# Kernel tuning notes

Hardware: AMD Instinct MI355X
Metric: run time of the kernel (lower is better)

## Reference

```python
import jax, jax.numpy as jnp
import numpy as np
from jax import lax

B, S, I = 256, 16, 64
D = 128
N_ITEMS = 100000
K = 3
PAD_ID = 0
BOS_ID = N_ITEMS
DILATIONS = (1, 2, 4)


def setup_inputs() -> dict:
    key = jax.random.key(0)
    ks = jax.random.split(key, 16)
    item_id = jax.random.randint(ks[0], (B, S, I), 0, N_ITEMS, dtype=jnp.int32)
    eval_from = jax.random.randint(ks[1], (B,), 0, S, dtype=jnp.int32)
    u_type = jax.random.randint(ks[2], (B,), 0, 4, dtype=jnp.int32)
    emb = jax.random.normal(ks[3], (N_ITEMS + 1, D), jnp.float32) * 0.05
    emb = emb.at[PAD_ID].set(0.0)  # padding_idx=0
    kaiming = (2.0 / (D * K)) ** 0.5
    conv_w0 = jax.random.normal(ks[4], (D, D, K), jnp.float32) * kaiming
    conv_w1 = jax.random.normal(ks[5], (D, D, K), jnp.float32) * kaiming
    conv_w2 = jax.random.normal(ks[6], (D, D, K), jnp.float32) * kaiming
    conv_b0 = jnp.zeros((D,), jnp.float32)
    conv_b1 = jnp.zeros((D,), jnp.float32)
    conv_b2 = jnp.zeros((D,), jnp.float32)
    gru_wih = jax.random.normal(ks[7], (3 * D, D), jnp.float32) * 0.05
    gru_whh = jax.random.normal(ks[8], (3 * D, D), jnp.float32) * 0.05
    gru_bih = jax.random.normal(ks[9], (3 * D,), jnp.float32) * 0.05
    gru_bhh = jax.random.normal(ks[10], (3 * D,), jnp.float32) * 0.05
    fus_w = jax.random.normal(ks[11], (D, 2 * D), jnp.float32) * 0.05
    fus_b = jnp.zeros((D,), jnp.float32)
    return {"item_id": item_id, "eval_from": eval_from, "u_type": u_type,
            "emb": emb,
            "conv_w0": conv_w0, "conv_b0": conv_b0,
            "conv_w1": conv_w1, "conv_b1": conv_b1,
            "conv_w2": conv_w2, "conv_b2": conv_b2,
            "gru_wih": gru_wih, "gru_whh": gru_whh,
            "gru_bih": gru_bih, "gru_bhh": gru_bhh,
            "fus_w": fus_w, "fus_b": fus_b}


def reference(item_id, eval_from, u_type, emb,
              conv_w0, conv_b0, conv_w1, conv_b1, conv_w2, conv_b2,
              gru_wih, gru_whh, gru_bih, gru_bhh, fus_w, fus_b):
    item_id = jnp.maximum(item_id, 0)  # clamp_min(0)
    Bc, Sc, Ic = item_id.shape
    convs = ((conv_w0, conv_b0, DILATIONS[0]),
             (conv_w1, conv_b1, DILATIONS[1]),
             (conv_w2, conv_b2, DILATIONS[2]))

    def tcn(x):  # x: [B, T, D] -> [B, T, D]
        h = jnp.transpose(x, (0, 2, 1))  # NCH
        for w, b, dil in convs:
            pad = (K - 1) * dil
            out = lax.conv_general_dilated(
                h, w, window_strides=(1,), padding=[(pad, 0)],
                rhs_dilation=(dil,),
                dimension_numbers=('NCH', 'OIH', 'NCH')) + b[None, :, None]
            h = jax.nn.relu(out + h)
        return jnp.transpose(h, (0, 2, 1))

    def gru_step(h, x):  # h,x: [B, D]
        gi = x @ gru_wih.T + gru_bih
        gh = h @ gru_whh.T + gru_bhh
        ir, iz, inn = jnp.split(gi, 3, axis=-1)
        hr, hz, hn = jnp.split(gh, 3, axis=-1)
        r = jax.nn.sigmoid(ir + hr)
        z = jax.nn.sigmoid(iz + hz)
        n = jnp.tanh(inn + r * hn)
        return (1.0 - z) * n + z * h

    pos = jnp.arange(Ic + 1)
    bos = jnp.full((Bc, 1), BOS_ID, dtype=item_id.dtype)

    def step(h, seq_s):  # seq_s: [B, I]
        lengths = (seq_s != PAD_ID).sum(-1)          # [B]
        max_len = lengths.max()                       # batch-level session max
        seq = jnp.concatenate([bos, seq_s], axis=1)   # [B, I+1], BOS prepended
        valid = pos[None, :] <= max_len               # positions torch keeps
        seq = jnp.where(valid, seq, PAD_ID)
        mask = seq != PAD_ID
        e = emb[seq]                                  # [B, I+1, D] (PAD row is 0)
        tc = tcn(e)
        fin = jnp.concatenate([tc, jnp.broadcast_to(h[:, None, :], tc.shape)], -1)
        reps = fin @ fus_w.T + fus_b                  # [B, I+1, D]
        reps = reps * valid[..., None]                # torch zero-pads beyond max_len
        # drop mask at last valid token (per-sample python loop in torch)
        mask = mask & ~((pos[None, :] == lengths[:, None]) & (lengths > 0)[:, None])
        mf = mask.astype(e.dtype)
        mean_emb = (e * mf[..., None]).sum(1) / jnp.maximum(mf.sum(1), 1.0)[:, None]
        h2 = gru_step(h, mean_emb)
        return h2, (reps, mask)

    h0 = jnp.zeros((Bc, D), jnp.float32)
    _, (reps, masks) = lax.scan(step, h0, jnp.transpose(item_id, (1, 0, 2)))
    reps = jnp.transpose(reps, (1, 0, 2, 3))          # [B, S, I+1, D]
    masks = jnp.transpose(masks, (1, 0, 2))           # [B, S, I+1]
    allow = jnp.arange(Sc)[None, :] >= eval_from[:, None]
    loss_masks = masks & allow[:, :, None]
    return reps, loss_masks, u_type
```

## Files before the change

### kernel.cpp

```cpp
#include <hip/hip_runtime.h>

#define BB 256
#define SS 16
#define II 64
#define DD 128
#define TT 65
#define BOS_ID 100000
#define XROW 256
#define XROWS 73
#define XT (XROWS*XROW)

#define OFF_LEN  0
#define OFF_ML   16384
#define OFF_ME   32768
#define OFF_HB   (32768 + 2097152)
#define OFF_WB2  (OFF_HB + 2097152)
#define OFF_WIHP (OFF_WB2 + 327680)
#define OFF_WGRU (OFF_WIHP + 98304)

#define OUT_MASK  (BB*SS*TT*DD)
#define OUT_UTYPE (OUT_MASK + BB*SS*TT)

typedef __attribute__((ext_vector_type(8))) short short8;
typedef __attribute__((ext_vector_type(4))) float f32x4;

__device__ __forceinline__ unsigned short f2bf(float f) {
    unsigned int u = __builtin_bit_cast(unsigned int, f);
    return (unsigned short)((u + 0x7fffu + ((u >> 16) & 1u)) >> 16);
}
__device__ __forceinline__ float bflo(unsigned int u) {
    return __builtin_bit_cast(float, u << 16);
}
__device__ __forceinline__ float bfhi(unsigned int u) {
    return __builtin_bit_cast(float, u & 0xffff0000u);
}
__device__ __forceinline__ void gld16(const void* g, void* l) {
    __builtin_amdgcn_global_load_lds(
        (const __attribute__((address_space(1))) void*)g,
        (__attribute__((address_space(3))) void*)l, 16, 0, 0);
}

__global__ __launch_bounds__(256) void prep_kernel(
    const float* __restrict__ w0, const float* __restrict__ w1,
    const float* __restrict__ w2, const float* __restrict__ fus_w,
    const float* __restrict__ wih, const float* __restrict__ whh,
    const int* __restrict__ item_id, const int* __restrict__ u_type,
    unsigned short* __restrict__ wB2,
    unsigned int* __restrict__ wih4, unsigned int* __restrict__ wgru4,
    int* __restrict__ lengths, int* __restrict__ maxlen,
    float* __restrict__ u_out)
{
    if (blockIdx.x >= 864) {
        int s = blockIdx.x - 864;
        int b = threadIdx.x;
        const int* row = item_id + (b * SS + s) * II;
        int cnt = 0;
        for (int i = 0; i < II; ++i) cnt += (row[i] > 0);
        lengths[b * SS + s] = cnt;
        __shared__ int red[256];
        red[b] = cnt;
        __syncthreads();
        for (int off = 128; off > 0; off >>= 1) {
            if (b < off) red[b] = max(red[b], red[b + off]);
            __syncthreads();
        }
        if (b == 0) maxlen[s] = red[0];
        if (s == 0) u_out[b] = (float)u_type[b];
        return;
    }
    int idx = blockIdx.x * 256 + threadIdx.x;
    if (idx < 163840) {
        int cid2  = idx >> 11;
        int inner = idx & 2047;
        int g = inner >> 9;
        int c = (inner >> 3) & 63;
        int e = inner & 7;
        int nh   = cid2 & 1;
        int rest = cid2 >> 1;
        int cq   = rest & 3;
        int m    = rest >> 2;
        int ci = cq * 32 + g * 8 + e;
        int co = nh * 64 + c;
        float v;
        if (m < 9) {
            int L = m / 3, k = m % 3;
            const float* w = (L == 0) ? w0 : ((L == 1) ? w1 : w2);
            v = w[(co * 128 + ci) * 3 + k];
            if (k == 2 && ci == co) v += 1.0f;
        } else {
            v = fus_w[co * 256 + ci];
        }
        wB2[idx] = f2bf(v);
    } else if (idx < 163840 + 24576) {
        int f   = idx - 163840;
        int dd4 = f / 1536;
        int rem = f - dd4 * 1536;
        int r   = rem >> 2;
        int c   = rem & 3;
        int d0  = 8 * dd4 + 2 * c;
        unsigned int lo = f2bf(wih[r * 128 + d0]);
        unsigned int hi = f2bf(wih[r * 128 + d0 + 1]);
        wih4[f] = (hi << 16) | lo;
    } else if (idx < 163840 + 24576 + 32768) {
        int f   = idx - 163840 - 24576;
        int dd4 = f >> 11;
        int rem = f & 2047;
        int r   = rem >> 2;
        int c   = rem & 3;
        int d0  = 8 * dd4 + 2 * c;
        float v0, v1;
        if (r < 384) { v0 = whh[r * 128 + d0]; v1 = whh[r * 128 + d0 + 1]; }
        else { const float* fw = fus_w + (r - 384) * 256 + 128;
               v0 = fw[d0]; v1 = fw[d0 + 1]; }
        wgru4[f] = ((unsigned int)f2bf(v1) << 16) | (unsigned int)f2bf(v0);
    }
}

__global__ __launch_bounds__(128) void mean_kernel(
    const int* __restrict__ item_id, const int* __restrict__ eval_from,
    const float* __restrict__ emb,
    const int* __restrict__ lengths, const int* __restrict__ maxlen,
    float* __restrict__ mean_emb, float* __restrict__ mask_out)
{
    int bid = blockIdx.x;
    int b = bid >> 4, s = bid & 15;
    int tid = threadIdx.x;
    __shared__ int seqs[TT];
    __shared__ int msk[TT];
    int ml  = maxlen[s];
    int len = lengths[bid];
    int ef  = eval_from[b];
    if (tid < TT) {
        int v;
        if (tid == 0) v = BOS_ID;
        else { int it = item_id[bid * II + tid - 1]; v = it > 0 ? it : 0; }
        if (tid > ml) v = 0;
        int m = (v != 0) && !(tid == len && len > 0);
        seqs[tid] = v;
        msk[tid]  = m;
        mask_out[bid * TT + tid] = (m && (s >= ef)) ? 1.0f : 0.0f;
    }
    __syncthreads();
    int cnt = 0;
    for (int p = 0; p < TT; ++p) cnt += msk[p];
    float acc = 0.0f;
    int d = tid;
    for (int p = 0; p < TT; ++p) {
        if (msk[p]) acc += emb[seqs[p] * DD + d];
    }
    mean_emb[bid * DD + d] = acc / (float)max(cnt, 1);
}

__global__ __launch_bounds__(512, 1) void gru_kernel(
    const float* __restrict__ me_all, const unsigned int* __restrict__ wih4,
    const float* __restrict__ bih,
    const unsigned int* __restrict__ wgru4, const float* __restrict__ bhh,
    const float* __restrict__ fus_b, float* __restrict__ hB)
{
    __shared__ __align__(16) unsigned int wl[16 * 384 * 4];
    __shared__ __align__(16) float me[2][DD];
    __shared__ unsigned int hpk[64];
    __shared__ float g_z[DD], g_inn[DD], g_hn[DD];
    int t = threadIdx.x;
    int b = blockIdx.x;
    int j = t & 127;
    int grp = t >> 7;

    {
        const unsigned char* g = (const unsigned char*)wih4 + t * 16;
        unsigned char* l = (unsigned char*)wl + t * 16;
#pragma unroll
        for (int i = 0; i < 12; ++i) gld16(g + i * 8192, l + i * 8192);
    }
    uint4 w[16];
    const uint4* wg4 = (const uint4*)wgru4;
#pragma unroll
    for (int dd4 = 0; dd4 < 16; ++dd4) w[dd4] = wg4[dd4 * 512 + t];

    float bias_hh = (t < 384) ? bhh[t] : fus_b[j];
    float bias_ih = (t < 384) ? bih[t] : 0.0f;
    if (t < DD) me[0][t] = me_all[b * SS * DD + t];
    float hj = 0.0f;
    if (t < 64) hpk[t] = 0u;
    asm volatile("s_waitcnt vmcnt(0)" ::: "memory");
    __syncthreads();

    const uint4* wl4 = (const uint4*)wl;
    for (int s = 0; s < SS; ++s) {
        if (t < DD && s < 15) me[(s + 1) & 1][t] = me_all[(b * SS + s + 1) * DD + t];
        const float* mc = me[s & 1];
        float gi = bias_ih;
        if (grp < 3) {
#pragma unroll
            for (int dd4 = 0; dd4 < 16; ++dd4) {
                uint4 u = wl4[dd4 * 384 + t];
                float4 m0 = *(const float4*)&mc[8 * dd4];
                float4 m1 = *(const float4*)&mc[8 * dd4 + 4];
                gi += bflo(u.x) * m0.x + bfhi(u.x) * m0.y;
                gi += bflo(u.y) * m0.z + bfhi(u.y) * m0.w;
                gi += bflo(u.z) * m1.x + bfhi(u.z) * m1.y;
                gi += bflo(u.w) * m1.z + bfhi(u.w) * m1.w;
            }
        }
        float acc = bias_hh;
#pragma unroll
        for (int dd4 = 0; dd4 < 16; ++dd4) {
            uint4 hp = *(const uint4*)&hpk[dd4 * 4];
            uint4 u  = w[dd4];
            acc += bflo(u.x) * bflo(hp.x) + bfhi(u.x) * bfhi(hp.x);
            acc += bflo(u.y) * bflo(hp.y) + bfhi(u.y) * bfhi(hp.y);
            acc += bflo(u.z) * bflo(hp.z) + bfhi(u.z) * bfhi(hp.z);
            acc += bflo(u.w) * bflo(hp.w) + bfhi(u.w) * bfhi(hp.w);
        }
        if (grp == 3) {
            hB[(s * BB + b) * DD + j] = acc;
        } else if (grp == 1) { g_z[j] = gi + acc; }
        else if (grp == 2)   { g_inn[j] = gi; g_hn[j] = acc; }
        __syncthreads();
        if (grp == 0) {
            float r = 1.0f / (1.0f + expf(-(gi + acc)));
            float z = 1.0f / (1.0f + expf(-g_z[j]));
            float n = tanhf(g_inn[j] + r * g_hn[j]);
            float hnew = (1.0f - z) * n + z * hj;
            hj = hnew;
            float hnb = __shfl_xor(hnew, 1);
            if ((j & 1) == 0) {
                unsigned int pk;
                asm("v_cvt_pk_bf16_f32 %0, %1, %2" : "=v"(pk) : "v"(hnew), "v"(hnb));
                hpk[j >> 1] = pk;
            }
        }
        __syncthreads();
    }
}

__global__ __launch_bounds__(256, 3) void tcn_kernel(
    const int* __restrict__ item_id, const float* __restrict__ emb,
    const int* __restrict__ maxlen,
    const unsigned short* __restrict__ wB2,
    const float* __restrict__ cb0, const float* __restrict__ cb1,
    const float* __restrict__ cb2,
    const float* __restrict__ hB, float* __restrict__ reps)
{
    __shared__ __align__(16) unsigned char lds_x[2][XT];
    __shared__ __align__(16) unsigned char ring[2][8192];

    const int tid = threadIdx.x, bid = blockIdx.x;
    const int lane = tid & 63, wv = tid >> 6;
    const int l15 = lane & 15, q4 = lane >> 4;
    const int t = wv >> 1, nh = wv & 1;
    const int tile = bid * 2 + t;
    const int b = tile >> 4, s = tile & 15;
    const int ml = maxlen[s];

    const unsigned char* wgbase = (const unsigned char*)wB2;
    unsigned char* xb = lds_x[t];

    {
        const unsigned char* src = wgbase + wv * 1024 + lane * 16;
        gld16(src,        &ring[0][wv * 1024]);
        gld16(src + 4096, &ring[0][4096 + wv * 1024]);
    }
    int* seqs2 = (int*)&ring[1][0];
    if (tid < 2 * TT) {
        int tt = tid / TT, p = tid - tt * TT;
        int tl = bid * 2 + tt;
        int v;
        if (p == 0) v = BOS_ID;
        else { int it = item_id[tl * II + p - 1]; v = it > 0 ? it : 0; }
        if (p > maxlen[tl & 15]) v = 0;
        seqs2[tt * TT + p] = v;
    }
    {
        float4 z = {0.f, 0.f, 0.f, 0.f};
        if (tid < 128) *(float4*)(lds_x[0] + tid * 16) = z;
        else           *(float4*)(lds_x[1] + (tid - 128) * 16) = z;
    }
    __syncthreads();

    for (int p = nh; p < TT; p += 2) {
        const float* er = emb + (long)seqs2[t * TT + p] * DD + lane * 2;
        float f0 = er[0], f1 = er[1];
        unsigned int pk = ((unsigned int)f2bf(f1) << 16) | (unsigned int)f2bf(f0);
        *(unsigned int*)(xb + (8 + p) * XROW + ((lane * 4) ^ ((p & 7) << 4))) = pk;
    }

    f32x4 acc[5][4];

#pragma unroll 1
    for (int cid = 0; cid < 40; ++cid) {
        int L = 0, cq, off, kq = 0;
        if (cid < 36) { L = cid / 12; kq = cid - L * 12; int k = kq >> 2; cq = kq & 3; off = (2 - k) << L; }
        else { cq = cid - 36; off = 0; }
        if (cid == 36 || (cid < 36 && kq == 0)) {
#pragma unroll
            for (int mt = 0; mt < 5; ++mt)
#pragma unroll
                for (int nt = 0; nt < 4; ++nt)
#pragma unroll
                    for (int r = 0; r < 4; ++r) acc[mt][nt][r] = 0.0f;
        }
        asm volatile("s_waitcnt vmcnt(0)" ::: "memory");
        __syncthreads();

        if (cid <= 38) {
            const unsigned char* src =
                wgbase + (size_t)(cid + 1) * 8192 + wv * 1024 + lane * 16;
            gld16(src,        &ring[(cid + 1) & 1][wv * 1024]);
            gld16(src + 4096, &ring[(cid + 1) & 1][4096 + wv * 1024]);
        }

        const unsigned char* sb = &ring[cid & 1][nh * 4096];
        const int xmask = ((l15 - off) & 7) << 4;
        const int colx  = (cq * 64 + q4 * 16) ^ xmask;
        short8 bfr[4], af[5];
#pragma unroll
        for (int nt = 0; nt < 4; ++nt)
            bfr[nt] = *(const short8*)(sb + q4 * 1024 + (nt * 16 + l15) * 16);
#pragma unroll
        for (int mt = 0; mt < 5; ++mt) {
            int rowA = 8 + mt * 16 + l15 - off;
            af[mt] = *(const short8*)(xb + rowA * XROW + colx);
        }
#pragma unroll
        for (int nt = 0; nt < 4; ++nt)
#pragma unroll
            for (int mt = 0; mt < 5; ++mt)
                acc[mt][nt] = __builtin_amdgcn_mfma_f32_16x16x32_bf16(
                    af[mt], bfr[nt], acc[mt][nt], 0, 0, 0);

        if (cid < 36 && kq == 11) {
            const float* cb = (L == 0) ? cb0 : ((L == 1) ? cb1 : cb2);
            __syncthreads();
#pragma unroll
            for (int nt = 0; nt < 4; ++nt) {
                float bia = cb[nh * 64 + nt * 16 + l15];
                int cbyte = nh * 128 + nt * 32 + l15 * 2;
#pragma unroll
                for (int mt = 0; mt < 5; ++mt)
#pragma unroll
                    for (int r = 0; r < 4; ++r) {
                        int p = mt * 16 + q4 * 4 + r;
                        if (p < TT) {
                            int row = 8 + p;
                            float v = acc[mt][nt][r] + bia;
                            *(unsigned short*)(xb + row * XROW +
                                               (cbyte ^ ((row & 7) << 4))) =
                                f2bf(v > 0.f ? v : 0.f);
                        }
                    }
            }
            __syncthreads();
        }
    }

    float hb[4];
#pragma unroll
    for (int nt = 0; nt < 4; ++nt)
        hb[nt] = hB[(s * BB + b) * DD + nh * 64 + nt * 16 + l15];
    long ob = (long)tile * (TT * DD);
#pragma unroll
    for (int mt = 0; mt < 5; ++mt)
#pragma unroll
        for (int nt = 0; nt < 4; ++nt)
#pragma unroll
            for (int r = 0; r < 4; ++r) {
                int p = mt * 16 + q4 * 4 + r;
                if (p < TT) {
                    float v = (p <= ml) ? (acc[mt][nt][r] + hb[nt]) : 0.0f;
                    reps[ob + p * DD + nh * 64 + nt * 16 + l15] = v;
                }
            }
}

extern "C" void kernel_launch(void* const* d_in, const int* in_sizes, int n_in,
                              void* d_out, int out_size, void* d_ws, size_t ws_size,
                              hipStream_t stream) {
    const int*   item_id   = (const int*)  d_in[0];
    const int*   eval_from = (const int*)  d_in[1];
    const int*   u_type    = (const int*)  d_in[2];
    const float* emb       = (const float*)d_in[3];
    const float* conv_w0   = (const float*)d_in[4];
    const float* conv_b0   = (const float*)d_in[5];
    const float* conv_w1   = (const float*)d_in[6];
    const float* conv_b1   = (const float*)d_in[7];
    const float* conv_w2   = (const float*)d_in[8];
    const float* conv_b2   = (const float*)d_in[9];
    const float* gru_wih   = (const float*)d_in[10];
    const float* gru_whh   = (const float*)d_in[11];
    const float* gru_bih   = (const float*)d_in[12];
    const float* gru_bhh   = (const float*)d_in[13];
    const float* fus_w     = (const float*)d_in[14];
    const float* fus_b     = (const float*)d_in[15];

    char* ws = (char*)d_ws;
    int*            lengths  = (int*)           (ws + OFF_LEN);
    int*            maxlen   = (int*)           (ws + OFF_ML);
    float*          mean_emb = (float*)         (ws + OFF_ME);
    float*          hB       = (float*)         (ws + OFF_HB);
    unsigned short* wB2      = (unsigned short*)(ws + OFF_WB2);
    unsigned int*   wih4     = (unsigned int*)  (ws + OFF_WIHP);
    unsigned int*   wgru4    = (unsigned int*)  (ws + OFF_WGRU);

    float* out  = (float*)d_out;
    float* reps = out;
    float* mout = out + OUT_MASK;
    float* uout = out + OUT_UTYPE;

    prep_kernel<<<880, 256, 0, stream>>>(conv_w0, conv_w1, conv_w2, fus_w,
                                         gru_wih, gru_whh, item_id, u_type,
                                         wB2, wih4, wgru4, lengths, maxlen, uout);
    mean_kernel<<<BB * SS, 128, 0, stream>>>(item_id, eval_from, emb, lengths, maxlen,
                                             mean_emb, mout);
    gru_kernel<<<BB, 512, 0, stream>>>(mean_emb, wih4, gru_bih,
                                       wgru4, gru_bhh, fus_b, hB);
    tcn_kernel<<<BB * SS / 2, 256, 0, stream>>>(item_id, emb, maxlen, wB2,
                                                conv_b0, conv_b1, conv_b2, hB, reps);
}
```

Measured before the change: 243.2 us.

## Double weight-chunk size in TCN pipeline and split mean gather across two thread groups

The TCN kernel now streams weights in 16 KB super-chunks covering two K-chunks each, which halves the number of barrier-plus-vmcnt waits per tile and processes two chunks of MFMAs between syncs. The larger ring buffer raises LDS use, so the occupancy hint drops from 3 to 2 blocks per CU. Separately, mean_kernel uses 256 threads that split the 65-position embedding gather between two halves and combine the partial sums through shared memory, which doubles memory-level parallelism on that gather. The trade is fewer resident TCN blocks and an extra barrier in the mean kernel.

```diff
diff --git a/kernel.cpp b/kernel.cpp
--- a/kernel.cpp
+++ b/kernel.cpp
@@ -116,7 +116,7 @@
     }
 }
 
-__global__ __launch_bounds__(128) void mean_kernel(
+__global__ __launch_bounds__(256) void mean_kernel(
     const int* __restrict__ item_id, const int* __restrict__ eval_from,
     const float* __restrict__ emb,
     const int* __restrict__ lengths, const int* __restrict__ maxlen,
@@ -125,8 +125,10 @@
     int bid = blockIdx.x;
     int b = bid >> 4, s = bid & 15;
     int tid = threadIdx.x;
+    int d = tid & 127, tg = tid >> 7;
     __shared__ int seqs[TT];
     __shared__ int msk[TT];
+    __shared__ float part[DD];
     int ml  = maxlen[s];
     int len = lengths[bid];
     int ef  = eval_from[b];
@@ -144,11 +146,13 @@
     int cnt = 0;
     for (int p = 0; p < TT; ++p) cnt += msk[p];
     float acc = 0.0f;
-    int d = tid;
-    for (int p = 0; p < TT; ++p) {
-        if (msk[p]) acc += emb[seqs[p] * DD + d];
-    }
-    mean_emb[bid * DD + d] = acc / (float)max(cnt, 1);
+    for (int p = tg; p < TT; p += 2) {
+        if (msk[p]) acc += emb[(long)seqs[p] * DD + d];
+    }
+    if (tg == 1) part[d] = acc;
+    __syncthreads();
+    if (tg == 0)
+        mean_emb[bid * DD + d] = (acc + part[d]) / (float)max(cnt, 1);
 }
 
 __global__ __launch_bounds__(512, 1) void gru_kernel(
@@ -234,7 +238,7 @@
     }
 }
 
-__global__ __launch_bounds__(256, 3) void tcn_kernel(
+__global__ __launch_bounds__(256, 2) void tcn_kernel(
     const int* __restrict__ item_id, const float* __restrict__ emb,
     const int* __restrict__ maxlen,
     const unsigned short* __restrict__ wB2,
@@ -243,7 +247,7 @@
     const float* __restrict__ hB, float* __restrict__ reps)
 {
     __shared__ __align__(16) unsigned char lds_x[2][XT];
-    __shared__ __align__(16) unsigned char ring[2][8192];
+    __shared__ __align__(16) unsigned char ring[2][16384];
 
     const int tid = threadIdx.x, bid = blockIdx.x;
     const int lane = tid & 63, wv = tid >> 6;
@@ -258,8 +262,10 @@
 
     {
         const unsigned char* src = wgbase + wv * 1024 + lane * 16;
-        gld16(src,        &ring[0][wv * 1024]);
-        gld16(src + 4096, &ring[0][4096 + wv * 1024]);
+        gld16(src,         &ring[0][wv * 1024]);
+        gld16(src + 4096,  &ring[0][4096 + wv * 1024]);
+        gld16(src + 8192,  &ring[0][8192 + wv * 1024]);
+        gld16(src + 12288, &ring[0][12288 + wv * 1024]);
     }
     int* seqs2 = (int*)&ring[1][0];
     if (tid < 2 * TT) {
@@ -288,11 +294,8 @@
     f32x4 acc[5][4];
 
 #pragma unroll 1
-    for (int cid = 0; cid < 40; ++cid) {
-        int L = 0, cq, off, kq = 0;
-        if (cid < 36) { L = cid / 12; kq = cid - L * 12; int k = kq >> 2; cq = kq & 3; off = (2 - k) << L; }
-        else { cq = cid - 36; off = 0; }
-        if (cid == 36 || (cid < 36 && kq == 0)) {
+    for (int sc = 0; sc < 20; ++sc) {
+        if (sc == 18 || (sc < 18 && sc % 6 == 0)) {
 #pragma unroll
             for (int mt = 0; mt < 5; ++mt)
 #pragma unroll
@@ -303,33 +306,44 @@
         asm volatile("s_waitcnt vmcnt(0)" ::: "memory");
         __syncthreads();
 
-        if (cid <= 38) {
+        if (sc <= 18) {
             const unsigned char* src =
-                wgbase + (size_t)(cid + 1) * 8192 + wv * 1024 + lane * 16;
-            gld16(src,        &ring[(cid + 1) & 1][wv * 1024]);
-            gld16(src + 4096, &ring[(cid + 1) & 1][4096 + wv * 1024]);
-        }
-
-        const unsigned char* sb = &ring[cid & 1][nh * 4096];
-        const int xmask = ((l15 - off) & 7) << 4;
-        const int colx  = (cq * 64 + q4 * 16) ^ xmask;
-        short8 bfr[4], af[5];
-#pragma unroll
-        for (int nt = 0; nt < 4; ++nt)
-            bfr[nt] = *(const short8*)(sb + q4 * 1024 + (nt * 16 + l15) * 16);
-#pragma unroll
-        for (int mt = 0; mt < 5; ++mt) {
-            int rowA = 8 + mt * 16 + l15 - off;
-            af[mt] = *(const short8*)(xb + rowA * XROW + colx);
-        }
-#pragma unroll
-        for (int nt = 0; nt < 4; ++nt)
-#pragma unroll
-            for (int mt = 0; mt < 5; ++mt)
-                acc[mt][nt] = __builtin_amdgcn_mfma_f32_16x16x32_bf16(
-                    af[mt], bfr[nt], acc[mt][nt], 0, 0, 0);
-
-        if (cid < 36 && kq == 11) {
+                wgbase + (size_t)(sc + 1) * 16384 + wv * 1024 + lane * 16;
+            unsigned char* dst = &ring[(sc + 1) & 1][0];
+            gld16(src,         dst + wv * 1024);
+            gld16(src + 4096,  dst + 4096 + wv * 1024);
+            gld16(src + 8192,  dst + 8192 + wv * 1024);
+            gld16(src + 12288, dst + 12288 + wv * 1024);
+        }
+
+#pragma unroll
+        for (int half = 0; half < 2; ++half) {
+            int cid = 2 * sc + half;
+            int L = 0, cq, off;
+            if (cid < 36) { L = cid / 12; int kq = cid - L * 12; int k = kq >> 2; cq = kq & 3; off = (2 - k) << L; }
+            else { cq = cid - 36; off = 0; }
+            const unsigned char* sb = &ring[sc & 1][half * 8192 + nh * 4096];
+            const int xmask = ((l15 - off) & 7) << 4;
+            const int colx  = (cq * 64 + q4 * 16) ^ xmask;
+            short8 bfr[4], af[5];
+#pragma unroll
+            for (int nt = 0; nt < 4; ++nt)
+                bfr[nt] = *(const short8*)(sb + q4 * 1024 + (nt * 16 + l15) * 16);
+#pragma unroll
+            for (int mt = 0; mt < 5; ++mt) {
+                int rowA = 8 + mt * 16 + l15 - off;
+                af[mt] = *(const short8*)(xb + rowA * XROW + colx);
+            }
+#pragma unroll
+            for (int nt = 0; nt < 4; ++nt)
+#pragma unroll
+                for (int mt = 0; mt < 5; ++mt)
+                    acc[mt][nt] = __builtin_amdgcn_mfma_f32_16x16x32_bf16(
+                        af[mt], bfr[nt], acc[mt][nt], 0, 0, 0);
+        }
+
+        if (sc < 18 && sc % 6 == 5) {
+            int L = sc / 6;
             const float* cb = (L == 0) ? cb0 : ((L == 1) ? cb1 : cb2);
             __syncthreads();
 #pragma unroll
@@ -410,7 +424,7 @@
     prep_kernel<<<880, 256, 0, stream>>>(conv_w0, conv_w1, conv_w2, fus_w,
                                          gru_wih, gru_whh, item_id, u_type,
                                          wB2, wih4, wgru4, lengths, maxlen, uout);
-    mean_kernel<<<BB * SS, 128, 0, stream>>>(item_id, eval_from, emb, lengths, maxlen,
+    mean_kernel<<<BB * SS, 256, 0, stream>>>(item_id, eval_from, emb, lengths, maxlen,
                                              mean_emb, mout);
     gru_kernel<<<BB, 512, 0, stream>>>(mean_emb, wih4, gru_bih,
                                        wgru4, gru_bhh, fus_b, hB);
```

New measurement: 235.9 us. 3.0% less time.
